# Kernel tuning notes

Hardware: AMD Instinct MI355X
Metric: run time of the kernel (lower is better)

Reference implementation:

```python
import jax, jax.numpy as jnp
import numpy as np
from jax import lax

C = 8          # bargs.channel
S = 1024       # bargs.test_sidelen
SIGMA = 1.0    # edge_sigma
KS = int(6 * SIGMA + 1)   # 7
PAD = KS // 2             # 3
BW = S // 6               # border_width
LAM, MU, TH = 5.0, 5.0, 1e-4


def _edge_kernel():
    coords = jnp.arange(KS, dtype=jnp.float32) - (KS - 1.0) / 2.0
    g1 = jnp.exp(-coords ** 2 / (2.0 * SIGMA ** 2))
    g1 = g1 / g1.sum()
    g2 = jnp.outer(g1, g1)
    return jnp.broadcast_to(g2, (C, 1, KS, KS))  # depthwise OIHW


def _alpha():
    # max applicable loop index among {row-dist, col-dist}; interior stays 1.
    r = jnp.arange(S)
    g = jnp.where(r < BW, r, jnp.where(S - 1 - r < BW, S - 1 - r, -1))  # [S]
    m = jnp.maximum(g[:, None], g[None, :])                              # [S,S]
    a = jnp.where(m >= 0, m.astype(jnp.float32) / BW, 1.0)
    return a[None, None]  # [1,1,S,S] broadcasts over channels


def _grad_spectrum():
    gv = jnp.array([[-1., -2., -1.], [0., 0., 0.], [1., 2., 1.]], jnp.float32)
    gh = gv.T
    gvf = jnp.fft.fft2(gv, s=(S, S))
    ghf = jnp.fft.fft2(gh, s=(S, S))
    return (jnp.abs(gvf) ** 2 + jnp.abs(ghf) ** 2).astype(jnp.float32)  # real


def _edge_blur(img, kernel, alpha):
    blurred = lax.conv_general_dilated(
        img, kernel, window_strides=(1, 1), padding=[(PAD, PAD), (PAD, PAD)],
        feature_group_count=C, dimension_numbers=('NCHW', 'OIHW', 'NCHW'))
    return alpha * img + (1.0 - alpha) * blurred


def setup_inputs() -> dict:
    key = jax.random.key(0)
    k1, k2 = jax.random.split(key)
    lms = jax.random.uniform(k1, (1, C, S, S), dtype=jnp.float32)
    fuse = jax.random.uniform(k2, (1, C, S, S), dtype=jnp.float32)
    return {"lms": lms, "fuse": fuse}


def reference(lms, fuse):
    kernel = _edge_kernel()
    alpha = _alpha()
    grad = _grad_spectrum()

    lms_fft = jnp.fft.fft2(_edge_blur(lms, kernel, alpha))
    fuse_fft = jnp.fft.fft2(_edge_blur(fuse, kernel, alpha))

    denom = jnp.abs(fuse_fft) ** 2 + LAM + MU * grad      # real [1,C,S,S]
    numer = jnp.conj(fuse_fft) * lms_fft
    psf = jnp.fft.fftshift(jnp.real(jnp.fft.ifft2(numer / denom)), axes=(-2, -1))
    psf = jnp.where(psf < TH, 0.0, psf)                   # [1,C,S,S]

    def crop(p):  # p: [S,S]
        row, col = jnp.unravel_index(jnp.argmax(p), p.shape)
        patch = lax.dynamic_slice(p, (row - 20, col - 20), (41, 41))
        return patch / jnp.sum(patch)

    psf_l = jax.vmap(crop)(psf[0])        # [C,41,41]
    return psf_l[:, None]                 # [C,1,41,41]
```

## Files before the change

kernel.cpp:

```cpp
#include <hip/hip_runtime.h>
#include <math.h>

#define SS 1024
#define NC 8
#define BWD 170
#define THRESH 1e-4f

typedef unsigned long long ull;

__device__ __forceinline__ float2 cmul(float2 a, float2 b) {
    return make_float2(a.x * b.x - a.y * b.y, a.x * b.y + a.y * b.x);
}

#define XS(a) ((a) ^ (((a) >> 4) & 15))

template <int DIRSIGN>
__device__ __forceinline__ void fft_fill_lut(float2* lut, int tid) {
    for (int i = tid; i < 768; i += 256) {
        float rev = (float)i * (1.0f / 1024.0f);
        float cv = __builtin_amdgcn_cosf(rev);
        float sv = __builtin_amdgcn_sinf(rev);
        lut[i] = make_float2(cv, (float)DIRSIGN * sv);
    }
}

template <int DIRSIGN>
__device__ __forceinline__ void bfly4(const float2 v[4], float2 r[4]) {
    float2 a = v[0], b = v[1], c = v[2], d = v[3];
    float2 apc = make_float2(a.x + c.x, a.y + c.y);
    float2 amc = make_float2(a.x - c.x, a.y - c.y);
    float2 bpd = make_float2(b.x + d.x, b.y + d.y);
    float2 jb  = make_float2(-(b.y - d.y), b.x - d.x);
    r[0] = make_float2(apc.x + bpd.x, apc.y + bpd.y);
    r[2] = make_float2(apc.x - bpd.x, apc.y - bpd.y);
    if (DIRSIGN == -1) {
        r[1] = make_float2(amc.x - jb.x, amc.y - jb.y);
        r[3] = make_float2(amc.x + jb.x, amc.y + jb.y);
    } else {
        r[1] = make_float2(amc.x + jb.x, amc.y + jb.y);
        r[3] = make_float2(amc.x - jb.x, amc.y - jb.y);
    }
}

template <int DIRSIGN, bool CONJ>
__device__ __forceinline__ void fft1024_reg(float2 v[4], float2* A, float2* B,
                                            const float2* lut, int tid) {
    float2* dst = A;
    float2* alt = B;
    #pragma unroll
    for (int t = 0; t < 4; ++t) {
        int s = 1 << (2 * t);
        int k = tid & ~(s - 1);
        float2 r[4];
        bfly4<DIRSIGN>(v, r);
        float2 w1 = lut[k], w2 = lut[2 * k], w3 = lut[3 * k];
        if (CONJ) { w1.y = -w1.y; w2.y = -w2.y; w3.y = -w3.y; }
        int base = tid + 3 * k;
        dst[XS(base)]         = r[0];
        dst[XS(base + s)]     = cmul(r[1], w1);
        dst[XS(base + 2 * s)] = cmul(r[2], w2);
        dst[XS(base + 3 * s)] = cmul(r[3], w3);
        __syncthreads();
        v[0] = dst[XS(tid)];
        v[1] = dst[XS(tid + 256)];
        v[2] = dst[XS(tid + 512)];
        v[3] = dst[XS(tid + 768)];
        float2* tmp = dst; dst = alt; alt = tmp;
    }
    float2 r[4];
    bfly4<DIRSIGN>(v, r);
    v[0] = r[0]; v[1] = r[1]; v[2] = r[2]; v[3] = r[3];
}

#define PIDX(r) ((r) + ((r) >> 5))

__global__ __launch_bounds__(256) void blur_fft_kernel(
        const float* __restrict__ lms, const float* __restrict__ fuse,
        float2* __restrict__ Zf) {
    __shared__ float2 bufA[1024];
    __shared__ float2 smemB2[1068];
    __shared__ float2 lut[768];
    float* rowl = (float*)smemB2;
    float* rowf = rowl + 1068;
    int tid = threadIdx.x;
    int g = blockIdx.x;
    int c = g >> 10;
    int y = (g & 7) * 128 + ((g >> 3) & 127);
    const float* L = lms + ((size_t)c << 20);
    const float* F = fuse + ((size_t)c << 20);
    int x0 = tid << 2;

    double e1 = exp(-0.5), e2 = exp(-2.0), e3 = exp(-4.5);
    double sm = 1.0 + 2.0 * (e1 + e2 + e3);
    float w[7] = { (float)(e3 / sm), (float)(e2 / sm), (float)(e1 / sm),
                   (float)(1.0 / sm),
                   (float)(e1 / sm), (float)(e2 / sm), (float)(e3 / sm) };

    bool rowInt = (y >= BWD) && (y <= SS - 1 - BWD);
    bool skipLoads = rowInt && (tid >= 45) && (tid <= 210);
    bool doH = !rowInt || (tid <= 43) || (tid >= 212);

    float4 cl, cf;
    if (skipLoads) {
        cl = *(const float4*)&L[((size_t)y << 10) + x0];
        cf = *(const float4*)&F[((size_t)y << 10) + x0];
    } else {
        float4 lv[7], fv[7];
        #pragma unroll
        for (int r = 0; r < 7; ++r) {
            int gy = y - 3 + r;
            if (gy >= 0 && gy < SS) {
                lv[r] = *(const float4*)&L[((size_t)gy << 10) + x0];
                fv[r] = *(const float4*)&F[((size_t)gy << 10) + x0];
            } else {
                lv[r] = make_float4(0.f, 0.f, 0.f, 0.f);
                fv[r] = make_float4(0.f, 0.f, 0.f, 0.f);
            }
        }
        cl = lv[3]; cf = fv[3];
        #pragma unroll
        for (int j = 0; j < 4; ++j) {
            float a = 0.f, b = 0.f;
            #pragma unroll
            for (int r = 0; r < 7; ++r) {
                a += w[r] * (&lv[r].x)[j];
                b += w[r] * (&fv[r].x)[j];
            }
            rowl[PIDX(3 + x0 + j)] = a;
            rowf[PIDX(3 + x0 + j)] = b;
        }
    }
    if (tid < 3) {
        rowl[PIDX(tid)] = 0.f; rowf[PIDX(tid)] = 0.f;
        rowl[PIDX(1027 + tid)] = 0.f; rowf[PIDX(1027 + tid)] = 0.f;
    }
    fft_fill_lut<-1>(lut, tid);
    __syncthreads();

    float bl[4] = {0.f, 0.f, 0.f, 0.f}, bf[4] = {0.f, 0.f, 0.f, 0.f};
    if (doH) {
        #pragma unroll
        for (int k = 0; k < 4; ++k) {
            float a = 0.f, b = 0.f;
            #pragma unroll
            for (int j = 0; j < 7; ++j) {
                a += w[j] * rowl[PIDX(x0 + k + j)];
                b += w[j] * rowf[PIDX(x0 + k + j)];
            }
            bl[k] = a; bf[k] = b;
        }
    }
    int gyv = (y < BWD) ? y : ((SS - 1 - y) < BWD ? (SS - 1 - y) : -1);
    #pragma unroll
    for (int k = 0; k < 4; ++k) {
        int x = x0 + k;
        int gx = (x < BWD) ? x : ((SS - 1 - x) < BWD ? (SS - 1 - x) : -1);
        int m = gyv > gx ? gyv : gx;
        float a = (m >= 0) ? (float)m / (float)BWD : 1.0f;
        bufA[XS(x)] = make_float2(a * (&cl.x)[k] + (1.0f - a) * bl[k],
                                  a * (&cf.x)[k] + (1.0f - a) * bf[k]);
    }
    __syncthreads();

    float2 v[4];
    #pragma unroll
    for (int m = 0; m < 4; ++m) v[m] = bufA[XS(tid + (m << 8))];
    fft1024_reg<-1, false>(v, smemB2, bufA, lut, tid);

    float2* Zrow = Zf + (((size_t)c << 20) + ((size_t)y << 10));
    #pragma unroll
    for (int r = 0; r < 4; ++r) Zrow[tid + (r << 8)] = v[r];
}

__global__ __launch_bounds__(256) void fft2_wiener_kernel(
        const float2* __restrict__ Z, float2* __restrict__ Wb) {
    __shared__ float2 resbuf[4][1024];
    __shared__ float2 scratch[1024];
    __shared__ float2 lut[768];
    int tid = threadIdx.x;
    int p = blockIdx.x >> 9;
    int i = blockIdx.x & 511;
    int rows[2];
    rows[0] = (i == 0) ? 0 : i;
    rows[1] = (i == 0) ? 512 : 1024 - i;
    bool selfp = (i == 0);

    fft_fill_lut<-1>(lut, tid);
    __syncthreads();

    float2 v[4], nv[4];
    {
        const float2* g0 = Z + (((size_t)(2 * p) << 20) +
                                ((size_t)rows[0] << 10));
        #pragma unroll
        for (int m = 0; m < 4; ++m) v[m] = g0[tid + (m << 8)];
    }
    #pragma unroll
    for (int combo = 0; combo < 4; ++combo) {
        if (combo < 3) {
            int nr = (combo + 1) >> 1, nc = (combo + 1) & 1;
            const float2* gn = Z + (((size_t)(2 * p + nc) << 20) +
                                    ((size_t)rows[nr] << 10));
            #pragma unroll
            for (int m = 0; m < 4; ++m) nv[m] = gn[tid + (m << 8)];
        }
        fft1024_reg<-1, false>(v, scratch, resbuf[combo], lut, tid);
        #pragma unroll
        for (int r = 0; r < 4; ++r)
            resbuf[combo][XS(tid + (r << 8))] = v[r];
        if (combo < 3) {
            #pragma unroll
            for (int m = 0; m < 4; ++m) v[m] = nv[m];
        }
    }
    __syncthreads();

    float2 gout[2][4];
    #pragma unroll
    for (int o = 0; o < 2; ++o) {
        int u = rows[o];
        int po = selfp ? o : (1 - o);
        float cu = __builtin_amdgcn_cosf((float)u * (1.0f / 1024.0f));
        float c2u = 2.0f * cu * cu - 1.0f;
        float hu = 2.0f + 2.0f * cu;
        #pragma unroll
        for (int j = 0; j < 4; ++j) {
            int vv = tid + (j << 8);
            int vn = (1024 - vv) & 1023;
            float cv = __builtin_amdgcn_cosf((float)vv * (1.0f / 1024.0f));
            float c2v = 2.0f * cv * cv - 1.0f;
            float hv = 2.0f + 2.0f * cv;
            float grad = (2.0f - 2.0f * c2v) * hu * hu +
                         (2.0f - 2.0f * c2u) * hv * hv;
            float regs = 5.0f + 5.0f * grad;
            float G0x, G0y, G1x, G1y;
            #pragma unroll
            for (int c = 0; c < 2; ++c) {
                float2 a = resbuf[o * 2 + c][XS(vv)];
                float2 b = resbuf[po * 2 + c][XS(vn)];
                float Lx = 0.5f * (a.x + b.x), Ly = 0.5f * (a.y - b.y);
                float Fx = 0.5f * (a.y + b.y), Fy = -0.5f * (a.x - b.x);
                float inv = 1.0f / (Fx * Fx + Fy * Fy + regs);
                float nx = (Fx * Lx + Fy * Ly) * inv;
                float ny = (Fx * Ly - Fy * Lx) * inv;
                if (c == 0) { G0x = nx; G0y = ny; } else { G1x = nx; G1y = ny; }
            }
            gout[o][j] = make_float2(G0x - G1y, G0y + G1x);
        }
    }
    __syncthreads();

    const float isc = 1.0f / 1024.0f;
    #pragma unroll
    for (int o = 0; o < 2; ++o) {
        float2 iv[4];
        #pragma unroll
        for (int j = 0; j < 4; ++j) iv[j] = gout[o][j];
        fft1024_reg<1, true>(iv, scratch, resbuf[o], lut, tid);
        float2* go = Wb + (((size_t)p << 20) + ((size_t)rows[o] << 10));
        #pragma unroll
        for (int r = 0; r < 4; ++r)
            go[tid + (r << 8)] = make_float2(iv[r].x * isc, iv[r].y * isc);
    }
}

__global__ __launch_bounds__(256) void ifft_final_kernel(
        const float2* __restrict__ Wd, float* __restrict__ psf,
        ull* __restrict__ bm) {
    __shared__ float2 bufA[1024];
    __shared__ float2 bufB[1024];
    __shared__ float2 lut[768];
    __shared__ ull red[256];
    int tid = threadIdx.x;
    const float2* g = Wd + ((size_t)blockIdx.x << 10);
    float2 v[4];
    #pragma unroll
    for (int m = 0; m < 4; ++m) v[m] = g[tid + (m << 8)];
    fft_fill_lut<1>(lut, tid);
    __syncthreads();
    fft1024_reg<1, false>(v, bufA, bufB, lut, tid);

    int p = blockIdx.x >> 10;
    int y = blockIdx.x & 1023;
    int oy = (y + 512) & 1023;
    float* p0 = psf + (((size_t)(2 * p) << 20) + ((size_t)oy << 10));
    float* p1 = p0 + (1u << 20);
    const float sc = 1.0f / 1024.0f;
    ull e0 = 0, e1 = 0;
    #pragma unroll
    for (int r = 0; r < 4; ++r) {
        int k = tid + (r << 8);
        float re = v[r].x * sc; re = (re < THRESH) ? 0.0f : re;
        float im = v[r].y * sc; im = (im < THRESH) ? 0.0f : im;
        int ox = (k + 512) & 1023;
        p0[ox] = re;
        p1[ox] = im;
        unsigned int idx = ((unsigned int)oy << 10) | (unsigned int)ox;
        ull c0 = ((ull)__float_as_uint(re) << 32) | (ull)(0xFFFFFFFFu - idx);
        ull c1 = ((ull)__float_as_uint(im) << 32) | (ull)(0xFFFFFFFFu - idx);
        e0 = c0 > e0 ? c0 : e0;
        e1 = c1 > e1 ? c1 : e1;
    }
    red[tid] = e0;
    __syncthreads();
    for (int s2 = 128; s2 > 0; s2 >>= 1) {
        if (tid < s2) { ull a = red[tid], b = red[tid + s2]; red[tid] = a > b ? a : b; }
        __syncthreads();
    }
    if (tid == 0) bm[((size_t)(2 * p) << 10) + y] = red[0];
    __syncthreads();
    red[tid] = e1;
    __syncthreads();
    for (int s2 = 128; s2 > 0; s2 >>= 1) {
        if (tid < s2) { ull a = red[tid], b = red[tid + s2]; red[tid] = a > b ? a : b; }
        __syncthreads();
    }
    if (tid == 0) bm[((size_t)(2 * p + 1) << 10) + y] = red[0];
}

__global__ __launch_bounds__(256) void transpose_kernel(float2* __restrict__ A) {
    __shared__ float2 ta[32][33];
    __shared__ float2 tb[32][33];
    float2* P = A + ((size_t)blockIdx.y << 20);
    int r = blockIdx.x, bi = 0;
    while (r >= 32 - bi) { r -= 32 - bi; ++bi; }
    int bj = bi + r;
    int tx = threadIdx.x & 31, ty = threadIdx.x >> 5;
    for (int yy = ty; yy < 32; yy += 8) {
        ta[yy][tx] = P[(size_t)(bi * 32 + yy) * SS + bj * 32 + tx];
        tb[yy][tx] = P[(size_t)(bj * 32 + yy) * SS + bi * 32 + tx];
    }
    __syncthreads();
    for (int yy = ty; yy < 32; yy += 8) {
        P[(size_t)(bi * 32 + yy) * SS + bj * 32 + tx] = tb[tx][yy];
        P[(size_t)(bj * 32 + yy) * SS + bi * 32 + tx] = ta[tx][yy];
    }
}

__global__ __launch_bounds__(256) void crop_kernel(
        const float* __restrict__ psf, const ull* __restrict__ bm,
        float* __restrict__ out) {
    int c = blockIdx.x;
    __shared__ ull rmax[256];
    __shared__ float red[256];
    int tid = threadIdx.x;
    ull e = 0;
    for (int i = tid; i < 1024; i += 256) {
        ull v = bm[((size_t)c << 10) + i];
        e = v > e ? v : e;
    }
    rmax[tid] = e;
    __syncthreads();
    for (int s2 = 128; s2 > 0; s2 >>= 1) {
        if (tid < s2) { ull a = rmax[tid], b = rmax[tid + s2]; rmax[tid] = a > b ? a : b; }
        __syncthreads();
    }
    unsigned int bidx = 0xFFFFFFFFu - (unsigned int)(rmax[0] & 0xFFFFFFFFull);
    int row = (int)(bidx >> 10), col = (int)(bidx & 1023);
    int r0 = row - 20; if (r0 < 0) r0 = 0; if (r0 > SS - 41) r0 = SS - 41;
    int c0 = col - 20; if (c0 < 0) c0 = 0; if (c0 > SS - 41) c0 = SS - 41;
    const float* p = psf + ((size_t)c << 20);
    float local = 0.0f;
    for (int i = tid; i < 1681; i += 256) {
        int rr = i / 41, cc = i - rr * 41;
        local += p[(size_t)(r0 + rr) * SS + c0 + cc];
    }
    red[tid] = local;
    __syncthreads();
    for (int s2 = 128; s2 > 0; s2 >>= 1) {
        if (tid < s2) red[tid] += red[tid + s2];
        __syncthreads();
    }
    float inv = 1.0f / red[0];
    for (int i = tid; i < 1681; i += 256) {
        int rr = i / 41, cc = i - rr * 41;
        out[c * 1681 + i] = p[(size_t)(r0 + rr) * SS + c0 + cc] * inv;
    }
}

extern "C" void kernel_launch(void* const* d_in, const int* in_sizes, int n_in,
                              void* d_out, int out_size, void* d_ws,
                              size_t ws_size, hipStream_t stream) {
    const float* lms = (const float*)d_in[0];
    const float* fuse = (const float*)d_in[1];
    char* ws = (char*)d_ws;
    float2* Zf = (float2*)ws;
    float2* Wb = (float2*)(ws + ((size_t)64 << 20));
    float* psf = (float*)ws;
    ull* bm = (ull*)(ws + ((size_t)33 << 20));
    float* outp = (float*)d_out;

    blur_fft_kernel<<<8192, 256, 0, stream>>>(lms, fuse, Zf);
    transpose_kernel<<<dim3(528, 8), 256, 0, stream>>>(Zf);
    fft2_wiener_kernel<<<2048, 256, 0, stream>>>(Zf, Wb);
    transpose_kernel<<<dim3(528, 4), 256, 0, stream>>>(Wb);
    ifft_final_kernel<<<4096, 256, 0, stream>>>(Wb, psf, bm);
    crop_kernel<<<8, 256, 0, stream>>>(psf, bm, outp);
}
```

Measured before the change: 215.1 us.

## Compute FFT twiddles in registers, use wave-shuffle reductions, vectorize transpose

Removes the shared-memory twiddle table and its fill and barrier in every kernel. Each stage now computes w1 with hardware sin/cos and derives w2 and w3 by complex multiplication. The ifft_final kernel replaces its two 8-step shared-memory tree reductions with 64-wide shuffle reductions plus a small cross-wave step. The in-place transpose now uses float4 global loads and stores. These cut LDS traffic, barriers and shared memory per block, which may raise occupancy, at the cost of extra ALU work and slightly different twiddle rounding.

```diff
diff --git a/kernel.cpp b/kernel.cpp
--- a/kernel.cpp
+++ b/kernel.cpp
@@ -14,17 +14,7 @@
 
 #define XS(a) ((a) ^ (((a) >> 4) & 15))
 
-template <int DIRSIGN>
-__device__ __forceinline__ void fft_fill_lut(float2* lut, int tid) {
-    for (int i = tid; i < 768; i += 256) {
-        float rev = (float)i * (1.0f / 1024.0f);
-        float cv = __builtin_amdgcn_cosf(rev);
-        float sv = __builtin_amdgcn_sinf(rev);
-        lut[i] = make_float2(cv, (float)DIRSIGN * sv);
-    }
-}
-
-template <int DIRSIGN>
+template <int DIR>
 __device__ __forceinline__ void bfly4(const float2 v[4], float2 r[4]) {
     float2 a = v[0], b = v[1], c = v[2], d = v[3];
     float2 apc = make_float2(a.x + c.x, a.y + c.y);
@@ -33,7 +23,7 @@
     float2 jb  = make_float2(-(b.y - d.y), b.x - d.x);
     r[0] = make_float2(apc.x + bpd.x, apc.y + bpd.y);
     r[2] = make_float2(apc.x - bpd.x, apc.y - bpd.y);
-    if (DIRSIGN == -1) {
+    if (DIR == -1) {
         r[1] = make_float2(amc.x - jb.x, amc.y - jb.y);
         r[3] = make_float2(amc.x + jb.x, amc.y + jb.y);
     } else {
@@ -42,9 +32,9 @@
     }
 }
 
-template <int DIRSIGN, bool CONJ>
+template <int DIR>
 __device__ __forceinline__ void fft1024_reg(float2 v[4], float2* A, float2* B,
-                                            const float2* lut, int tid) {
+                                            int tid) {
     float2* dst = A;
     float2* alt = B;
     #pragma unroll
@@ -52,9 +42,12 @@
         int s = 1 << (2 * t);
         int k = tid & ~(s - 1);
         float2 r[4];
-        bfly4<DIRSIGN>(v, r);
-        float2 w1 = lut[k], w2 = lut[2 * k], w3 = lut[3 * k];
-        if (CONJ) { w1.y = -w1.y; w2.y = -w2.y; w3.y = -w3.y; }
+        bfly4<DIR>(v, r);
+        float rev = (float)k * (1.0f / 1024.0f);
+        float2 w1 = make_float2(__builtin_amdgcn_cosf(rev),
+                                (float)DIR * __builtin_amdgcn_sinf(rev));
+        float2 w2 = cmul(w1, w1);
+        float2 w3 = cmul(w2, w1);
         int base = tid + 3 * k;
         dst[XS(base)]         = r[0];
         dst[XS(base + s)]     = cmul(r[1], w1);
@@ -68,7 +61,7 @@
         float2* tmp = dst; dst = alt; alt = tmp;
     }
     float2 r[4];
-    bfly4<DIRSIGN>(v, r);
+    bfly4<DIR>(v, r);
     v[0] = r[0]; v[1] = r[1]; v[2] = r[2]; v[3] = r[3];
 }
 
@@ -79,7 +72,6 @@
         float2* __restrict__ Zf) {
     __shared__ float2 bufA[1024];
     __shared__ float2 smemB2[1068];
-    __shared__ float2 lut[768];
     float* rowl = (float*)smemB2;
     float* rowf = rowl + 1068;
     int tid = threadIdx.x;
@@ -134,7 +126,6 @@
         rowl[PIDX(tid)] = 0.f; rowf[PIDX(tid)] = 0.f;
         rowl[PIDX(1027 + tid)] = 0.f; rowf[PIDX(1027 + tid)] = 0.f;
     }
-    fft_fill_lut<-1>(lut, tid);
     __syncthreads();
 
     float bl[4] = {0.f, 0.f, 0.f, 0.f}, bf[4] = {0.f, 0.f, 0.f, 0.f};
@@ -165,7 +156,7 @@
     float2 v[4];
     #pragma unroll
     for (int m = 0; m < 4; ++m) v[m] = bufA[XS(tid + (m << 8))];
-    fft1024_reg<-1, false>(v, smemB2, bufA, lut, tid);
+    fft1024_reg<-1>(v, smemB2, bufA, tid);
 
     float2* Zrow = Zf + (((size_t)c << 20) + ((size_t)y << 10));
     #pragma unroll
@@ -176,7 +167,6 @@
         const float2* __restrict__ Z, float2* __restrict__ Wb) {
     __shared__ float2 resbuf[4][1024];
     __shared__ float2 scratch[1024];
-    __shared__ float2 lut[768];
     int tid = threadIdx.x;
     int p = blockIdx.x >> 9;
     int i = blockIdx.x & 511;
@@ -185,9 +175,6 @@
     rows[1] = (i == 0) ? 512 : 1024 - i;
     bool selfp = (i == 0);
 
-    fft_fill_lut<-1>(lut, tid);
-    __syncthreads();
-
     float2 v[4], nv[4];
     {
         const float2* g0 = Z + (((size_t)(2 * p) << 20) +
@@ -204,7 +191,7 @@
             #pragma unroll
             for (int m = 0; m < 4; ++m) nv[m] = gn[tid + (m << 8)];
         }
-        fft1024_reg<-1, false>(v, scratch, resbuf[combo], lut, tid);
+        fft1024_reg<-1>(v, scratch, resbuf[combo], tid);
         #pragma unroll
         for (int r = 0; r < 4; ++r)
             resbuf[combo][XS(tid + (r << 8))] = v[r];
@@ -256,7 +243,7 @@
         float2 iv[4];
         #pragma unroll
         for (int j = 0; j < 4; ++j) iv[j] = gout[o][j];
-        fft1024_reg<1, true>(iv, scratch, resbuf[o], lut, tid);
+        fft1024_reg<1>(iv, scratch, resbuf[o], tid);
         float2* go = Wb + (((size_t)p << 20) + ((size_t)rows[o] << 10));
         #pragma unroll
         for (int r = 0; r < 4; ++r)
@@ -269,16 +256,14 @@
         ull* __restrict__ bm) {
     __shared__ float2 bufA[1024];
     __shared__ float2 bufB[1024];
-    __shared__ float2 lut[768];
-    __shared__ ull red[256];
+    __shared__ ull red0[4];
+    __shared__ ull red1[4];
     int tid = threadIdx.x;
     const float2* g = Wd + ((size_t)blockIdx.x << 10);
     float2 v[4];
     #pragma unroll
     for (int m = 0; m < 4; ++m) v[m] = g[tid + (m << 8)];
-    fft_fill_lut<1>(lut, tid);
-    __syncthreads();
-    fft1024_reg<1, false>(v, bufA, bufB, lut, tid);
+    fft1024_reg<1>(v, bufA, bufB, tid);
 
     int p = blockIdx.x >> 10;
     int y = blockIdx.x & 1023;
@@ -301,21 +286,25 @@
         e0 = c0 > e0 ? c0 : e0;
         e1 = c1 > e1 ? c1 : e1;
     }
-    red[tid] = e0;
-    __syncthreads();
-    for (int s2 = 128; s2 > 0; s2 >>= 1) {
-        if (tid < s2) { ull a = red[tid], b = red[tid + s2]; red[tid] = a > b ? a : b; }
-        __syncthreads();
-    }
-    if (tid == 0) bm[((size_t)(2 * p) << 10) + y] = red[0];
-    __syncthreads();
-    red[tid] = e1;
-    __syncthreads();
-    for (int s2 = 128; s2 > 0; s2 >>= 1) {
-        if (tid < s2) { ull a = red[tid], b = red[tid + s2]; red[tid] = a > b ? a : b; }
-        __syncthreads();
-    }
-    if (tid == 0) bm[((size_t)(2 * p + 1) << 10) + y] = red[0];
+    #pragma unroll
+    for (int off = 32; off > 0; off >>= 1) {
+        ull o0 = __shfl_down(e0, off);
+        ull o1 = __shfl_down(e1, off);
+        e0 = o0 > e0 ? o0 : e0;
+        e1 = o1 > e1 ? o1 : e1;
+    }
+    if ((tid & 63) == 0) { red0[tid >> 6] = e0; red1[tid >> 6] = e1; }
+    __syncthreads();
+    if (tid == 0) {
+        ull m0 = red0[0], m1 = red1[0];
+        #pragma unroll
+        for (int i2 = 1; i2 < 4; ++i2) {
+            m0 = red0[i2] > m0 ? red0[i2] : m0;
+            m1 = red1[i2] > m1 ? red1[i2] : m1;
+        }
+        bm[((size_t)(2 * p) << 10) + y] = m0;
+        bm[((size_t)(2 * p + 1) << 10) + y] = m1;
+    }
 }
 
 __global__ __launch_bounds__(256) void transpose_kernel(float2* __restrict__ A) {
@@ -325,15 +314,28 @@
     int r = blockIdx.x, bi = 0;
     while (r >= 32 - bi) { r -= 32 - bi; ++bi; }
     int bj = bi + r;
-    int tx = threadIdx.x & 31, ty = threadIdx.x >> 5;
-    for (int yy = ty; yy < 32; yy += 8) {
-        ta[yy][tx] = P[(size_t)(bi * 32 + yy) * SS + bj * 32 + tx];
-        tb[yy][tx] = P[(size_t)(bj * 32 + yy) * SS + bi * 32 + tx];
-    }
-    __syncthreads();
-    for (int yy = ty; yy < 32; yy += 8) {
-        P[(size_t)(bi * 32 + yy) * SS + bj * 32 + tx] = tb[tx][yy];
-        P[(size_t)(bj * 32 + yy) * SS + bi * 32 + tx] = ta[tx][yy];
+    int tx = threadIdx.x & 15;
+    int ty = threadIdx.x >> 4;
+    #pragma unroll
+    for (int yy0 = 0; yy0 < 32; yy0 += 16) {
+        int yy = yy0 + ty;
+        float4 va = *(const float4*)&P[(size_t)(bi * 32 + yy) * SS + bj * 32 + 2 * tx];
+        float4 vb = *(const float4*)&P[(size_t)(bj * 32 + yy) * SS + bi * 32 + 2 * tx];
+        ta[yy][2 * tx]     = make_float2(va.x, va.y);
+        ta[yy][2 * tx + 1] = make_float2(va.z, va.w);
+        tb[yy][2 * tx]     = make_float2(vb.x, vb.y);
+        tb[yy][2 * tx + 1] = make_float2(vb.z, vb.w);
+    }
+    __syncthreads();
+    #pragma unroll
+    for (int yy0 = 0; yy0 < 32; yy0 += 16) {
+        int yy = yy0 + ty;
+        float2 a0 = tb[2 * tx][yy], a1 = tb[2 * tx + 1][yy];
+        *(float4*)&P[(size_t)(bi * 32 + yy) * SS + bj * 32 + 2 * tx] =
+            make_float4(a0.x, a0.y, a1.x, a1.y);
+        float2 b0 = ta[2 * tx][yy], b1 = ta[2 * tx + 1][yy];
+        *(float4*)&P[(size_t)(bj * 32 + yy) * SS + bi * 32 + 2 * tx] =
+            make_float4(b0.x, b0.y, b1.x, b1.y);
     }
 }
 
```

Result: faster. 208.4 us (-3.1%).
